# Optimization experiments

Hardware: AMD Instinct MI355X
Metric: run time of the kernel (lower is better)

## Reference

```python
import jax, jax.numpy as jnp
import numpy as np


def setup_inputs() -> dict:
    key = jax.random.key(0)
    k1, k2 = jax.random.split(key)
    B, Cin, H, W = 8, 64, 256, 256
    Cout, K = 3, 7
    x = jax.random.normal(k1, (B, Cin, H, W), dtype=jnp.float32)
    d = jax.random.normal(k2, (B, Cout, Cin, K, K), dtype=jnp.float32)
    return {"x": x, "d": d}


def _per_sample_conv(xi, di):
    # xi: [Cin, Hp, Wp] (already circularly padded), di: [Cout, Cin, K, K]
    # 'VALID' conv reproduces torch conv2d on the padded input.
    out = jax.lax.conv_general_dilated(
        xi[None], di, window_strides=(1, 1), padding='VALID',
        dimension_numbers=('NCHW', 'OIHW', 'NCHW'))
    return out[0]  # [Cout, H, W]


def reference(x, d):
    # x: [B, Cin, H, W]; d: [B, Cout, Cin, K, K]
    pad = (d.shape[-1] - 1) // 2
    # F.pad(mode='circular') == jnp.pad(mode='wrap') on spatial dims
    xp = jnp.pad(x, ((0, 0), (0, 0), (pad, pad), (pad, pad)), mode='wrap')
    # sample_wise=True: each batch element uses its own filter bank
    y = jax.vmap(_per_sample_conv)(xp, d)  # [B, Cout, H, W]
    return y
```

## Files before the change

### kernel.cpp

```cpp
#include <hip/hip_runtime.h>
#include <hip/hip_bf16.h>
#include <stdint.h>


constexpr int NB = 8, CIN = 64, HH = 256, WW = 256, CO = 3, KK = 7;
constexpr int R = 8;
constexpr int XROWS = 14;
constexpr int CI_CHUNK = 8;
constexpr int NCH = CIN / CI_CHUNK;
constexpr int XBUF = XROWS * 256 * 8;

typedef short bf16x8 __attribute__((ext_vector_type(8)));
typedef float f32x16 __attribute__((ext_vector_type(16)));

__device__ inline uint16_t f2bf(float f) {
    union { __hip_bfloat16 h; uint16_t u; } cv;
    cv.h = __float2bfloat16(f);
    return cv.u;
}
__device__ inline int uswz(int u) { return u ^ ((u >> 4) & 15); }

__global__ __launch_bounds__(1024, 4)
void conv_mfma_v9(const float* __restrict__ x, const float* __restrict__ d,
                  float* __restrict__ outp) {
    __shared__ char smem[2 * XBUF * 2 + 32 * 64 * 8 * 2];
    uint16_t* Xl  = (uint16_t*)smem;
    uint16_t* Bl  = (uint16_t*)(smem + 2 * XBUF * 2);
    float*    tmp = (float*)smem;

    const int tid  = threadIdx.x;
    const int lane = tid & 63, wv = tid >> 6;
    const int y_t  = wv >> 1, xh = wv & 1;
    const int l31  = lane & 31, lh = lane >> 5;

    const int blk = blockIdx.x;
    const int b   = blk & 7;
    const int y0  = (blk >> 3) * R;

    const float* xb = x + (size_t)b * CIN * HH * WW;
    const float* db = d + (size_t)b * CO * CIN * KK * KK;

    f32x16 acc[4];
    #pragma unroll
    for (int m = 0; m < 4; ++m)
        #pragma unroll
        for (int i = 0; i < 16; ++i) acc[m][i] = 0.f;

    auto stageX = [&](int c, int buf) {
        if (tid < XROWS * 64) {
            const int r = tid >> 6, q = tid & 63;
            const int row = (y0 + r - 3) & (HH - 1);
            const float* p = xb + ((size_t)(c * CI_CHUNK) * HH + row) * WW + q * 4;
            float4 v[8];
            #pragma unroll
            for (int j = 0; j < 8; ++j)
                v[j] = *reinterpret_cast<const float4*>(p + (size_t)j * HH * WW);
            uint16_t* dst = Xl + (size_t)buf * XBUF + (size_t)r * 256 * 8;
            #pragma unroll
            for (int t = 0; t < 4; ++t) {
                uint4 pk;
                pk.x = (uint32_t)f2bf(((const float*)&v[0])[t]) | ((uint32_t)f2bf(((const float*)&v[1])[t]) << 16);
                pk.y = (uint32_t)f2bf(((const float*)&v[2])[t]) | ((uint32_t)f2bf(((const float*)&v[3])[t]) << 16);
                pk.z = (uint32_t)f2bf(((const float*)&v[4])[t]) | ((uint32_t)f2bf(((const float*)&v[5])[t]) << 16);
                pk.w = (uint32_t)f2bf(((const float*)&v[6])[t]) | ((uint32_t)f2bf(((const float*)&v[7])[t]) << 16);
                const int us = uswz(q * 4 + t);
                *reinterpret_cast<uint4*>(dst + (size_t)us * 8) = pk;
            }
        }
    };

    auto compute = [&](int c, int buf) {
        const uint16_t* Xb = Xl + (size_t)buf * XBUF;
        #pragma unroll
        for (int ks = 0; ks < 4; ++ks) {
            const int ky = ks * 2 + lh;
            int r = y_t + ky;
            if (r >= XROWS) r = 0;
            const int fi = c * 4 + ks;
            const bf16x8 bfrag = *reinterpret_cast<const bf16x8*>(&Bl[(size_t)(fi * 64 + lane) * 8]);
            #pragma unroll
            for (int m = 0; m < 4; ++m) {
                const int us = uswz(xh * 128 + m * 32 + l31);
                const bf16x8 afrag = *reinterpret_cast<const bf16x8*>(&Xb[((size_t)r * 256 + us) * 8]);
                acc[m] = __builtin_amdgcn_mfma_f32_32x32x16_bf16(afrag, bfrag, acc[m], 0, 0, 0);
            }
        }
    };

    stageX(0, 0);
    #pragma unroll
    for (int q2 = 0; q2 < 2; ++q2) {
        const int s = tid + q2 * 1024;
        const int fi = s >> 6, ln = s & 63;
        const int cc8 = fi >> 2, ks = fi & 3;
        const int h = ln >> 5, n = ln & 31;
        const int ky = ks * 2 + h, co = n >> 3, kx = n & 7;
        uint16_t vals[8];
        #pragma unroll
        for (int j = 0; j < 8; ++j) {
            float v = 0.f;
            if (co < CO && kx < KK && ky < KK)
                v = db[((size_t)co * CIN + cc8 * 8 + j) * (KK * KK) + ky * KK + kx];
            vals[j] = f2bf(v);
        }
        uint4 pk;
        pk.x = (uint32_t)vals[0] | ((uint32_t)vals[1] << 16);
        pk.y = (uint32_t)vals[2] | ((uint32_t)vals[3] << 16);
        pk.z = (uint32_t)vals[4] | ((uint32_t)vals[5] << 16);
        pk.w = (uint32_t)vals[6] | ((uint32_t)vals[7] << 16);
        *reinterpret_cast<uint4*>(&Bl[(size_t)(fi * 64 + ln) * 8]) = pk;
    }

    for (int c = 0; c < NCH; ++c) {
        __syncthreads();
        if (c + 1 < NCH) stageX(c + 1, (c + 1) & 1);
        compute(c, c & 1);
    }

    for (int p = 0; p < 2; ++p) {
        __syncthreads();
        if ((y_t >> 2) == p) {
            const int rr = y_t & 3;
            #pragma unroll
            for (int m = 0; m < 4; ++m)
                #pragma unroll
                for (int reg = 0; reg < 16; ++reg) {
                    const int rowloc = (reg & 3) + 8 * (reg >> 2) + 4 * lh;
                    const int u = xh * 128 + m * 32 + rowloc;
                    tmp[((size_t)rr * 256 + u) * 33 + l31] = acc[m][reg];
                }
        }
        __syncthreads();
        #pragma unroll
        for (int it0 = 0; it0 < 3; ++it0) {
            const int it = tid + it0 * 1024;
            if (it < 4 * CO * 256) {
                const int rr  = it / (CO * 256);
                const int rem = it - rr * (CO * 256);
                const int co  = rem >> 8, x0 = rem & 255;
                float s = 0.f;
                #pragma unroll
                for (int kx = 0; kx < 7; ++kx)
                    s += tmp[((size_t)rr * 256 + ((x0 + kx - 3) & 255)) * 33 + co * 8 + kx];
                outp[(((size_t)b * CO + co) * HH + (y0 + p * 4 + rr)) * WW + x0] = s;
            }
        }
    }
}

extern "C" void kernel_launch(void* const* d_in, const int* in_sizes, int n_in,
                              void* d_out, int out_size, void* d_ws, size_t ws_size,
                              hipStream_t stream) {
    const float* x = (const float*)d_in[0];
    const float* d = (const float*)d_in[1];
    float* outp = (float*)d_out;
    conv_mfma_v9<<<dim3(NB * (HH / R)), 1024, 0, stream>>>(x, d, outp);
}
```

Baseline: 39.05 us.

## Restructure MFMA conv so each A fragment feeds several output rows across ky

Each wave now owns one 32-column strip and four output rows. Every loaded input-row A fragment is reused across all output rows it contributes to (the ky fan-out), so each wave issues 10 LDS reads per chunk instead of one per MFMA. The channel chunk doubles to 16, filling the MFMA K dimension in one step and halving the number of chunks, and all seven ky filter fragments are held in registers. Double buffering is dropped in favour of a single buffer with an extra barrier, so global loads no longer overlap compute, which could expose load latency.

Measured after the change: 43.31 us. 10.9% more time.

```diff
diff --git a/kernel.cpp b/kernel.cpp
--- a/kernel.cpp
+++ b/kernel.cpp
@@ -6,9 +6,11 @@
 constexpr int NB = 8, CIN = 64, HH = 256, WW = 256, CO = 3, KK = 7;
 constexpr int R = 8;
 constexpr int XROWS = 14;
-constexpr int CI_CHUNK = 8;
-constexpr int NCH = CIN / CI_CHUNK;
-constexpr int XBUF = XROWS * 256 * 8;
+constexpr int CIC = 16;
+constexpr int NCH = CIN / CIC;
+constexpr int XLBYTES = XROWS * 256 * CIC * 2;
+constexpr int NBF = KK * NCH;
+constexpr int SMEMSZ = XLBYTES + NBF * 64 * 16;
 
 typedef short bf16x8 __attribute__((ext_vector_type(8)));
 typedef float f32x16 __attribute__((ext_vector_type(16)));
@@ -21,16 +23,16 @@
 __device__ inline int uswz(int u) { return u ^ ((u >> 4) & 15); }
 
 __global__ __launch_bounds__(1024, 4)
-void conv_mfma_v9(const float* __restrict__ x, const float* __restrict__ d,
-                  float* __restrict__ outp) {
-    __shared__ char smem[2 * XBUF * 2 + 32 * 64 * 8 * 2];
-    uint16_t* Xl  = (uint16_t*)smem;
-    uint16_t* Bl  = (uint16_t*)(smem + 2 * XBUF * 2);
+void conv_kyfan(const float* __restrict__ x, const float* __restrict__ d,
+                float* __restrict__ outp) {
+    __shared__ char smem[SMEMSZ];
+    uint16_t* Bl  = (uint16_t*)(smem + XLBYTES);
     float*    tmp = (float*)smem;
 
     const int tid  = threadIdx.x;
     const int lane = tid & 63, wv = tid >> 6;
-    const int y_t  = wv >> 1, xh = wv & 1;
+    const int m    = wv & 7;
+    const int rg   = wv >> 3;
     const int l31  = lane & 31, lh = lane >> 5;
 
     const int blk = blockIdx.x;
@@ -42,92 +44,102 @@
 
     f32x16 acc[4];
     #pragma unroll
-    for (int m = 0; m < 4; ++m)
+    for (int o = 0; o < 4; ++o)
         #pragma unroll
-        for (int i = 0; i < 16; ++i) acc[m][i] = 0.f;
+        for (int i = 0; i < 16; ++i) acc[o][i] = 0.f;
 
-    auto stageX = [&](int c, int buf) {
-        if (tid < XROWS * 64) {
-            const int r = tid >> 6, q = tid & 63;
-            const int row = (y0 + r - 3) & (HH - 1);
-            const float* p = xb + ((size_t)(c * CI_CHUNK) * HH + row) * WW + q * 4;
-            float4 v[8];
-            #pragma unroll
-            for (int j = 0; j < 8; ++j)
-                v[j] = *reinterpret_cast<const float4*>(p + (size_t)j * HH * WW);
-            uint16_t* dst = Xl + (size_t)buf * XBUF + (size_t)r * 256 * 8;
-            #pragma unroll
-            for (int t = 0; t < 4; ++t) {
-                uint4 pk;
-                pk.x = (uint32_t)f2bf(((const float*)&v[0])[t]) | ((uint32_t)f2bf(((const float*)&v[1])[t]) << 16);
-                pk.y = (uint32_t)f2bf(((const float*)&v[2])[t]) | ((uint32_t)f2bf(((const float*)&v[3])[t]) << 16);
-                pk.z = (uint32_t)f2bf(((const float*)&v[4])[t]) | ((uint32_t)f2bf(((const float*)&v[5])[t]) << 16);
-                pk.w = (uint32_t)f2bf(((const float*)&v[6])[t]) | ((uint32_t)f2bf(((const float*)&v[7])[t]) << 16);
-                const int us = uswz(q * 4 + t);
-                *reinterpret_cast<uint4*>(dst + (size_t)us * 8) = pk;
+    auto stageX = [&](int c) {
+        #pragma unroll
+        for (int k = 0; k < 2; ++k) {
+            const int it = tid + k * 1024;
+            if (it < XROWS * 128) {
+                const int r = it >> 7, rem = it & 127;
+                const int q = rem >> 1, h = rem & 1;
+                const int row = (y0 + r - 3) & (HH - 1);
+                const float* p = xb + ((size_t)(c * CIC + h * 8) * HH + row) * WW + q * 4;
+                float4 v[8];
+                #pragma unroll
+                for (int j = 0; j < 8; ++j)
+                    v[j] = *reinterpret_cast<const float4*>(p + (size_t)j * HH * WW);
+                #pragma unroll
+                for (int t = 0; t < 4; ++t) {
+                    uint4 pk;
+                    pk.x = (uint32_t)f2bf(((const float*)&v[0])[t]) | ((uint32_t)f2bf(((const float*)&v[1])[t]) << 16);
+                    pk.y = (uint32_t)f2bf(((const float*)&v[2])[t]) | ((uint32_t)f2bf(((const float*)&v[3])[t]) << 16);
+                    pk.z = (uint32_t)f2bf(((const float*)&v[4])[t]) | ((uint32_t)f2bf(((const float*)&v[5])[t]) << 16);
+                    pk.w = (uint32_t)f2bf(((const float*)&v[6])[t]) | ((uint32_t)f2bf(((const float*)&v[7])[t]) << 16);
+                    const int us = uswz(q * 4 + t);
+                    *reinterpret_cast<uint4*>(smem + ((size_t)r * 256 + us) * 32 + h * 16) = pk;
+                }
             }
         }
     };
 
-    auto compute = [&](int c, int buf) {
-        const uint16_t* Xb = Xl + (size_t)buf * XBUF;
+    auto compute = [&](int c) {
+        bf16x8 bf[KK];
         #pragma unroll
-        for (int ks = 0; ks < 4; ++ks) {
-            const int ky = ks * 2 + lh;
-            int r = y_t + ky;
-            if (r >= XROWS) r = 0;
-            const int fi = c * 4 + ks;
-            const bf16x8 bfrag = *reinterpret_cast<const bf16x8*>(&Bl[(size_t)(fi * 64 + lane) * 8]);
+        for (int ky = 0; ky < KK; ++ky)
+            bf[ky] = *reinterpret_cast<const bf16x8*>(&Bl[(size_t)((ky * NCH + c) * 64 + lane) * 8]);
+        const int ubase = uswz(m * 32 + l31) * 32 + lh * 16;
+        #pragma unroll
+        for (int r = 0; r < 10; ++r) {
+            const bf16x8 a = *reinterpret_cast<const bf16x8*>(
+                smem + ((size_t)(4 * rg + r) * 256) * 32 + ubase);
             #pragma unroll
-            for (int m = 0; m < 4; ++m) {
-                const int us = uswz(xh * 128 + m * 32 + l31);
-                const bf16x8 afrag = *reinterpret_cast<const bf16x8*>(&Xb[((size_t)r * 256 + us) * 8]);
-                acc[m] = __builtin_amdgcn_mfma_f32_32x32x16_bf16(afrag, bfrag, acc[m], 0, 0, 0);
+            for (int o = 0; o < 4; ++o) {
+                const int ky = r - o;
+                if (ky < 0 || ky >= KK) continue;
+                acc[o] = __builtin_amdgcn_mfma_f32_32x32x16_bf16(a, bf[ky], acc[o], 0, 0, 0);
             }
         }
     };
 
-    stageX(0, 0);
+    stageX(0);
     #pragma unroll
-    for (int q2 = 0; q2 < 2; ++q2) {
-        const int s = tid + q2 * 1024;
-        const int fi = s >> 6, ln = s & 63;
-        const int cc8 = fi >> 2, ks = fi & 3;
-        const int h = ln >> 5, n = ln & 31;
-        const int ky = ks * 2 + h, co = n >> 3, kx = n & 7;
-        uint16_t vals[8];
-        #pragma unroll
-        for (int j = 0; j < 8; ++j) {
-            float v = 0.f;
-            if (co < CO && kx < KK && ky < KK)
-                v = db[((size_t)co * CIN + cc8 * 8 + j) * (KK * KK) + ky * KK + kx];
-            vals[j] = f2bf(v);
+    for (int k = 0; k < 2; ++k) {
+        const int s = tid + k * 1024;
+        if (s < NBF * 64) {
+            const int fi = s >> 6, ln = s & 63;
+            const int ky = fi >> 2, ch = fi & 3;
+            const int n = ln & 31, lh2 = ln >> 5;
+            const int co = n >> 3, kx = n & 7;
+            uint16_t vals[8];
+            #pragma unroll
+            for (int j = 0; j < 8; ++j) {
+                const int ci = ch * CIC + lh2 * 8 + j;
+                float v = 0.f;
+                if (co < CO && kx < KK)
+                    v = db[((size_t)co * CIN + ci) * (KK * KK) + ky * KK + kx];
+                vals[j] = f2bf(v);
+            }
+            uint4 pk;
+            pk.x = (uint32_t)vals[0] | ((uint32_t)vals[1] << 16);
+            pk.y = (uint32_t)vals[2] | ((uint32_t)vals[3] << 16);
+            pk.z = (uint32_t)vals[4] | ((uint32_t)vals[5] << 16);
+            pk.w = (uint32_t)vals[6] | ((uint32_t)vals[7] << 16);
+            *reinterpret_cast<uint4*>(&Bl[(size_t)(fi * 64 + ln) * 8]) = pk;
         }
-        uint4 pk;
-        pk.x = (uint32_t)vals[0] | ((uint32_t)vals[1] << 16);
-        pk.y = (uint32_t)vals[2] | ((uint32_t)vals[3] << 16);
-        pk.z = (uint32_t)vals[4] | ((uint32_t)vals[5] << 16);
-        pk.w = (uint32_t)vals[6] | ((uint32_t)vals[7] << 16);
-        *reinterpret_cast<uint4*>(&Bl[(size_t)(fi * 64 + ln) * 8]) = pk;
     }
 
     for (int c = 0; c < NCH; ++c) {
         __syncthreads();
-        if (c + 1 < NCH) stageX(c + 1, (c + 1) & 1);
-        compute(c, c & 1);
+        compute(c);
+        if (c + 1 < NCH) {
+            __syncthreads();
+            stageX(c + 1);
+        }
     }
 
     for (int p = 0; p < 2; ++p) {
         __syncthreads();
-        if ((y_t >> 2) == p) {
-            const int rr = y_t & 3;
+        if (rg == p) {
             #pragma unroll
-            for (int m = 0; m < 4; ++m)
+            for (int o = 0; o < 4; ++o)
                 #pragma unroll
                 for (int reg = 0; reg < 16; ++reg) {
                     const int rowloc = (reg & 3) + 8 * (reg >> 2) + 4 * lh;
-                    const int u = xh * 128 + m * 32 + rowloc;
-                    tmp[((size_t)rr * 256 + u) * 33 + l31] = acc[m][reg];
+                    const int u = m * 32 + rowloc;
+                    tmp[((size_t)o * 256 + u) * 33 + l31] = acc[o][reg];
                 }
         }
         __syncthreads();
@@ -154,5 +166,5 @@
     const float* x = (const float*)d_in[0];
     const float* d = (const float*)d_in[1];
     float* outp = (float*)d_out;
-    conv_mfma_v9<<<dim3(NB * (HH / R)), 1024, 0, stream>>>(x, d, outp);
+    conv_kyfan<<<dim3(NB * (HH / R)), 1024, 0, stream>>>(x, d, outp);
 }
```
